# Performance work log

Hardware: AMD Instinct MI355X
Metric: run time of the kernel (lower is better)

## Reference

```python
import jax, jax.numpy as jnp
import numpy as np

# CUBA-LIF constants (from LavaNetwork.__init__ with beta=0.95)
THRESHOLD = 1.0
CURRENT_DECAY = 1.0   # current[t] = (1-1.0)*current[t-1] + input[t] == input[t]
VOLTAGE_DECAY = 1.0 - 0.95  # = 0.05, so v[t] = 0.95*v[t-1] + cur[t]

N_INPUT, N_HIDDEN, N_OUTPUT = 512, 2048, 4 * 64
B, T = 32, 1024


def setup_inputs() -> dict:
    key = jax.random.key(0)
    kx, k1, k2, k3, k4 = jax.random.split(key, 5)
    x = (jax.random.uniform(kx, (B, N_INPUT, T)) < 0.1).astype(jnp.float32)
    # learned params (Linear with bias); small scale so spiking is reasonable
    w1 = jax.random.normal(k1, (N_HIDDEN, N_INPUT), dtype=jnp.float32) * (1.0 / np.sqrt(N_INPUT))
    b1 = jax.random.normal(k2, (N_HIDDEN,), dtype=jnp.float32) * 0.01
    w2 = jax.random.normal(k3, (N_OUTPUT, N_HIDDEN), dtype=jnp.float32) * (1.0 / np.sqrt(N_HIDDEN))
    b2 = jax.random.normal(k4, (N_OUTPUT,), dtype=jnp.float32) * 0.01
    return {"x": x, "w1": w1, "b1": b1, "w2": w2, "b2": b2}


def _cuba_lif(cur):
    """CUBA neuron with current_decay=1 (current==synaptic input),
    leaky-integrate voltage, fire at threshold, reset voltage to 0.
    cur: (B, N, T) -> spikes (B, N, T)."""
    beta_v = 1.0 - VOLTAGE_DECAY  # 0.95

    def step(v, c_t):
        v = v * beta_v + c_t
        s = (v >= THRESHOLD).astype(v.dtype)
        v = v * (1.0 - s)  # reset-to-zero on spike (Loihi behavior)
        return v, s

    cur_t = jnp.moveaxis(cur, -1, 0)  # (T, B, N)
    v0 = jnp.zeros(cur.shape[:-1], cur.dtype)
    _, spk = jax.lax.scan(step, v0, cur_t)
    return jnp.moveaxis(spk, 0, -1)  # (B, N, T)


def reference(x, w1, b1, w2, b2):
    # layer 1: synapse (einsum 'bit,oi->bot' + bias) -> CUBA neuron
    cur1 = jnp.einsum('bit,oi->bot', x, w1) + b1[None, :, None]
    spk1 = _cuba_lif(cur1)
    # layer 2
    cur2 = jnp.einsum('bit,oi->bot', spk1, w2) + b2[None, :, None]
    spk2 = _cuba_lif(cur2)
    return (spk1, spk2)
```

## Files before the change

### kernel.cpp

```cpp
#include <hip/hip_runtime.h>


typedef int i32x4 __attribute__((ext_vector_type(4)));
typedef _Float16 f16x8 __attribute__((ext_vector_type(8)));
typedef _Float16 f16x4 __attribute__((ext_vector_type(4)));
typedef float f32x4 __attribute__((ext_vector_type(4)));

#define GLDS(g, l) __builtin_amdgcn_global_load_lds( \
    (const __attribute__((address_space(1))) void*)(g), \
    (__attribute__((address_space(3))) void*)(l), 16, 0, 0)

#define INV231 4.656612873077392578125e-10


__global__ __launch_bounds__(256) void prep_w8(const float* __restrict__ A,
                                               signed char* __restrict__ wp,
                                               int M, int K)
{
    long gt = (long)blockIdx.x * 256 + threadIdx.x;
    int kq4 = K >> 2;
    int m = (int)(gt / kq4), kq = (int)(gt % kq4);
    int k0 = kq * 4;
    int kt = k0 >> 6, kin = k0 & 63;
    int cw = ((kin >> 4) ^ (m >> 1)) & 3;
    float4 w = *(const float4*)&A[(long)m * K + k0];
    float wv[4] = {w.x, w.y, w.z, w.w};
    int pack[4] = {0, 0, 0, 0};
#pragma unroll
    for (int e = 0; e < 4; e++) {
        long k64 = (long)rint((double)wv[e] * 2147483648.0);
#pragma unroll
        for (int j = 0; j < 3; j++) {
            long r = ((k64 + 128) & 255) - 128;
            pack[j] |= ((int)r & 255) << (e * 8);
            k64 = (k64 - r) >> 8;
        }
        pack[3] |= ((int)k64 & 255) << (e * 8);
    }
#pragma unroll
    for (int p = 0; p < 4; p++)
        *(int*)&wp[(((long)kt * 4 + p) * M + m) * 64 + cw * 16 + (kin & 15)] = pack[p];
}

__global__ __launch_bounds__(256) void prep_x8(const float* __restrict__ x,
                                               unsigned char* __restrict__ xt)
{
    __shared__ float xs[64][68];
    const int b = blockIdx.z, i0 = blockIdx.y * 64, t0 = blockIdx.x * 64;
    const float* xb = x + ((long)b * 512 + i0) * 1024 + t0;
#pragma unroll
    for (int p = 0; p < 4; p++) {
        int f = threadIdx.x + p * 256;
        int i = f >> 4, t4 = (f & 15) * 4;
        *(float4*)&xs[i][t4] = *(const float4*)&xb[(long)i * 1024 + t4];
    }
    __syncthreads();
    int tt = threadIdx.x >> 2, c = threadIdx.x & 3;
    unsigned char bytes[16];
#pragma unroll
    for (int j = 0; j < 16; j++)
        bytes[j] = (unsigned char)xs[c * 16 + j][tt];
    *(uint4*)&xt[(((long)b * 8 + (i0 >> 6)) * 1024 + t0 + tt) * 64 + c * 16] =
        *(uint4*)bytes;
}

__global__ __launch_bounds__(192, 2) void gemm_lif1(
    const signed char* __restrict__ wp,
    const unsigned char* __restrict__ act,
    const float* __restrict__ bias,
    unsigned* __restrict__ mask_ws)
{
    __shared__ signed char Ws[8][4][16][64];
    __shared__ float cs[2][128][17];

    const int m0 = blockIdx.x * 16, b = blockIdx.y;
    const int tid = threadIdx.x, lane = tid & 63, wave = tid >> 6;
    const int lm = lane & 15, lq = lane >> 4;
    const int fro = ((lq ^ (lm >> 1)) & 3) * 16;
    const unsigned char* ab = act + (long)b * 8 * 1024 * 64;

    i32x4 areg[2][4];
    double bv0 = 0.0;

    if (wave < 2) {
        const int gl_row = lane >> 2, gl_col = (lane & 3) * 16;
#pragma unroll
        for (int j = 0; j < 16; ++j) {
            const int r = wave + 2 * j;
            const int kt = r >> 2, p = r & 3;
            const signed char* g = wp + ((long)r * 2048 + m0 + gl_row) * 64 + gl_col;
            GLDS(g, &Ws[kt][p][0][0]);
        }
        bv0 = (double)bias[m0 + lm];
#pragma unroll
        for (int f = 0; f < 4; f++)
            areg[0][f] = *(const i32x4*)
                &ab[((long)(wave * 64 + f * 16 + lm)) * 64 + lq * 16];
    }
    __syncthreads();

    double u = 0.0;
    bool sprev = false;

    for (int p = 0; p < 9; ++p) {
        if (wave < 2 && p < 8) {
            i32x4 acc[4][4];
#pragma unroll
            for (int pp = 0; pp < 4; pp++)
#pragma unroll
                for (int f = 0; f < 4; f++) acc[pp][f] = (i32x4)0;

#pragma unroll
            for (int kk = 0; kk < 8; ++kk) {
                {
                    int pn = p, kn = kk + 1;
                    if (kn == 8) { kn = 0; pn = p + 1; if (pn > 7) { pn = 7; kn = 7; } }
                    const long tt = (long)pn * 128 + wave * 64 + lm;
#pragma unroll
                    for (int f = 0; f < 4; f++)
                        areg[(kk + 1) & 1][f] = *(const i32x4*)
                            &ab[((long)kn * 1024 + tt + f * 16) * 64 + lq * 16];
                }
#pragma unroll
                for (int pp = 0; pp < 4; pp++) {
                    i32x4 w0 = *(const i32x4*)&Ws[kk][pp][lm][fro];
#pragma unroll
                    for (int f = 0; f < 4; f++)
                        acc[pp][f] = __builtin_amdgcn_mfma_i32_16x16x64_i8(
                            areg[kk & 1][f], w0, acc[pp][f], 0, 0, 0);
                }
            }
            const int tb = wave * 64;
#pragma unroll
            for (int tf = 0; tf < 4; tf++)
#pragma unroll
                for (int r = 0; r < 4; r++) {
                    long T = acc[3][tf][r];
                    T = T * 256 + acc[2][tf][r];
                    T = T * 256 + acc[1][tf][r];
                    T = T * 256 + acc[0][tf][r];
                    cs[p & 1][tb + tf * 16 + lq * 4 + r][lm] =
                        (float)((double)T * INV231 + bv0);
                }
        }
        if (wave == 2 && p >= 1 && lane < 16) {
            const int pq = p - 1, buf = pq & 1;
#pragma unroll 1
            for (int g = 0; g < 4; ++g) {
                unsigned mword = 0;
#pragma unroll
                for (int j = 0; j < 32; ++j) {
                    double c = (double)cs[buf][g * 32 + j][lane];
                    double a = 0.95 * u + c;
                    u = sprev ? c : a;
                    bool s = (u >= 1.0);
                    mword |= (s ? 1u : 0u) << j;
                    sprev = s;
                }
                mask_ws[((long)b * 32 + pq * 4 + g) * 2048 + m0 + lane] = mword;
            }
        }
        __syncthreads();
    }
}


__global__ __launch_bounds__(256) void expand_spk8(
    const unsigned* __restrict__ mask_ws,
    unsigned char* __restrict__ spk8)
{
    __shared__ unsigned msk[64][33];
    const int b = blockIdx.x, kt = blockIdx.y;
    const int tid = threadIdx.x;
#pragma unroll
    for (int i = 0; i < 8; ++i) {
        int idx = tid + i * 256;
        int tw = idx >> 6, m = idx & 63;
        msk[m][tw] = mask_ws[((long)b * 32 + tw) * 2048 + kt * 64 + m];
    }
    __syncthreads();
    unsigned char* dst = spk8 + ((long)b * 32 + kt) * 1024 * 64;
#pragma unroll
    for (int i = 0; i < 16; ++i) {
        int off = tid + i * 256;
        int t = off >> 2, mq = off & 3;
        int tw = t >> 5, sh = t & 31;
        unsigned w0 = 0, w1 = 0, w2 = 0, w3 = 0;
#pragma unroll
        for (int j = 0; j < 4; ++j) {
            w0 |= ((msk[mq * 16 + j][tw] >> sh) & 1u) << (8 * j);
            w1 |= ((msk[mq * 16 + 4 + j][tw] >> sh) & 1u) << (8 * j);
            w2 |= ((msk[mq * 16 + 8 + j][tw] >> sh) & 1u) << (8 * j);
            w3 |= ((msk[mq * 16 + 12 + j][tw] >> sh) & 1u) << (8 * j);
        }
        *(uint4*)&dst[(long)off * 16] = (uint4){w0, w1, w2, w3};
    }
}

__global__ __launch_bounds__(256) void expand_spk(
    const unsigned* __restrict__ mask_ws,
    float* __restrict__ spk1)
{
    __shared__ unsigned msk[8][32];
    const long rowbase = (long)blockIdx.x * 8;
    const int b = (int)(rowbase >> 11), m0 = (int)(rowbase & 2047);
    const int tid = threadIdx.x;
    {
        int w = tid >> 3, r = tid & 7;
        msk[r][w] = mask_ws[((long)b * 32 + w) * 2048 + m0 + r];
    }
    __syncthreads();
    const int r = tid >> 5, l5 = tid & 31;
    float* dst = spk1 + (rowbase + r) * 1024;
    const int sh = (l5 & 7) * 4;
#pragma unroll
    for (int j = 0; j < 8; j++) {
        const int t = l5 * 4 + j * 128;
        const unsigned w = msk[r][(l5 >> 3) + j * 4];
        float4 o;
        o.x = ((w >> sh) & 1u) ? 1.f : 0.f;
        o.y = ((w >> (sh + 1)) & 1u) ? 1.f : 0.f;
        o.z = ((w >> (sh + 2)) & 1u) ? 1.f : 0.f;
        o.w = ((w >> (sh + 3)) & 1u) ? 1.f : 0.f;
        *(float4*)&dst[t] = o;
    }
}

template <bool TRANS, int NITER, int CHUNK>
__global__ __launch_bounds__(256, 2) void gemm_i8(
    const signed char* __restrict__ wp,
    const unsigned char* __restrict__ act,
    const float* __restrict__ bias,
    float* __restrict__ C,
    int M)
{
    constexpr int NCHUNK = NITER / CHUNK;
    __shared__ signed char Ws[CHUNK][4][32][64];

    const int b = blockIdx.y;
    const int m0 = blockIdx.z * 32, t0 = blockIdx.x * 256;
    const int tid = threadIdx.x, lane = tid & 63, wave = tid >> 6;
    const int wt = t0 + wave * 64;
    const int lm = lane & 15, lq = lane >> 4;
    const int fro = ((lq ^ (lm >> 1)) & 3) * 16;
    const int gl_row = lane >> 2, gl_col = (lane & 3) * 16;

    const unsigned char* ab = act + (long)b * NITER * 1024 * 64;

    auto stage = [&](int cc) {
#pragma unroll
        for (int j = 0; j < CHUNK; ++j) {
            const int r = wave + 4 * j;
            const int kt = r >> 2, p = r & 3;
            const long kg = ((long)(cc * CHUNK + kt) * 4 + p);
            const signed char* g = wp + (kg * M + m0 + gl_row) * 64 + gl_col;
            GLDS(g, &Ws[kt][p][0][0]);
            GLDS(g + 16 * 64, &Ws[kt][p][16][0]);
        }
    };

    i32x4 acc[4][8];
#pragma unroll
    for (int p = 0; p < 4; p++)
#pragma unroll
        for (int q = 0; q < 8; q++) acc[p][q] = (i32x4)0;

    stage(0);
    i32x4 areg[2][4];
#pragma unroll
    for (int f = 0; f < 4; f++)
        areg[0][f] = *(const i32x4*)&ab[((long)(wt + f * 16 + lm)) * 64 + lq * 16];
    __syncthreads();

    for (int c = 0; c < NCHUNK; ++c) {
#pragma unroll
        for (int kk = 0; kk < CHUNK; ++kk) {
            {
                const int itv = c * CHUNK + kk;
                const long nx = (itv + 1 < NITER) ? itv + 1 : itv;
#pragma unroll
                for (int f = 0; f < 4; f++)
                    areg[(kk + 1) & 1][f] = *(const i32x4*)
                        &ab[(nx * 1024 + wt + f * 16 + lm) * 64 + lq * 16];
            }
#pragma unroll
            for (int p = 0; p < 4; p++) {
                i32x4 w0 = *(const i32x4*)&Ws[kk][p][lm][fro];
                i32x4 w1 = *(const i32x4*)&Ws[kk][p][16 + lm][fro];
                if (TRANS) {
#pragma unroll
                    for (int f = 0; f < 4; f++) {
                        acc[p][f * 2 + 0] = __builtin_amdgcn_mfma_i32_16x16x64_i8(
                            areg[kk & 1][f], w0, acc[p][f * 2 + 0], 0, 0, 0);
                        acc[p][f * 2 + 1] = __builtin_amdgcn_mfma_i32_16x16x64_i8(
                            areg[kk & 1][f], w1, acc[p][f * 2 + 1], 0, 0, 0);
                    }
                } else {
#pragma unroll
                    for (int f = 0; f < 4; f++) {
                        acc[p][0 + f] = __builtin_amdgcn_mfma_i32_16x16x64_i8(
                            w0, areg[kk & 1][f], acc[p][0 + f], 0, 0, 0);
                        acc[p][4 + f] = __builtin_amdgcn_mfma_i32_16x16x64_i8(
                            w1, areg[kk & 1][f], acc[p][4 + f], 0, 0, 0);
                    }
                }
            }
        }
        if (c + 1 < NCHUNK) {
            __syncthreads();
            stage(c + 1);
            __syncthreads();
        }
    }

    if (TRANS) {
        double bv[2];
        bv[0] = (double)bias[m0 + lm];
        bv[1] = (double)bias[m0 + 16 + lm];
        float* Cb = C + (long)b * 1024 * M;
#pragma unroll
        for (int tf = 0; tf < 4; tf++)
#pragma unroll
            for (int r = 0; r < 4; r++) {
                const int trow = wt + tf * 16 + lq * 4 + r;
#pragma unroll
                for (int mf = 0; mf < 2; mf++) {
                    long T = acc[3][tf * 2 + mf][r];
                    T = T * 256 + acc[2][tf * 2 + mf][r];
                    T = T * 256 + acc[1][tf * 2 + mf][r];
                    T = T * 256 + acc[0][tf * 2 + mf][r];
                    Cb[(long)trow * M + m0 + mf * 16 + lm] =
                        (float)((double)T * INV231 + bv[mf]);
                }
            }
    } else {
        float* Cb = C + (long)b * M * 1024;
#pragma unroll
        for (int mf = 0; mf < 2; mf++)
#pragma unroll
            for (int r = 0; r < 4; r++) {
                const int mrow = m0 + mf * 16 + lq * 4 + r;
                const double bv = (double)bias[mrow];
#pragma unroll
                for (int tf = 0; tf < 4; tf++) {
                    long T = acc[3][mf * 4 + tf][r];
                    T = T * 256 + acc[2][mf * 4 + tf][r];
                    T = T * 256 + acc[1][mf * 4 + tf][r];
                    T = T * 256 + acc[0][mf * 4 + tf][r];
                    Cb[(long)mrow * 1024 + wt + tf * 16 + lm] =
                        (float)((double)T * INV231 + bv);
                }
            }
    }
}

template <int RPB>
__global__ __launch_bounds__(256) void lif_lds(float* __restrict__ cur)
{
    __shared__ float cs[RPB][36];
    const long rowbase = (long)blockIdx.x * RPB;
    float* base = cur + rowbase * 1024;
    const int tid = threadIdx.x;
    double v = 0.0;
    const int NV = RPB * 32 / 4;
    for (int tc = 0; tc < 1024; tc += 32) {
        for (int f = tid; f < NV; f += 256) {
            int row = f >> 3, t4 = (f & 7) * 4;
            *(float4*)&cs[row][t4] = *(const float4*)&base[(long)row * 1024 + tc + t4];
        }
        __syncthreads();
        if (tid < RPB) {
#pragma unroll
            for (int j = 0; j < 32; j++) {
                v = 0.95 * v + (double)cs[tid][j];
                bool s = v >= 1.0;
                cs[tid][j] = s ? 1.f : 0.f;
                if (s) v = 0.0;
            }
        }
        __syncthreads();
        for (int f = tid; f < NV; f += 256) {
            int row = f >> 3, t4 = (f & 7) * 4;
            *(float4*)&base[(long)row * 1024 + tc + t4] = *(float4*)&cs[row][t4];
        }
        __syncthreads();
    }
}


__device__ inline void split3(float w, _Float16& q0, _Float16& q1, _Float16& q2) {
    float p0 = rintf(w * 4096.f) * 2.44140625e-4f;
    float r1 = w - p0;
    float p1s = rintf(r1 * 8388608.f) * 2.44140625e-4f;
    float r2 = r1 - p1s * 4.8828125e-4f;
    float p2s = rintf(r2 * 1.7179869184e10f) * 1.220703125e-4f;
    q0 = (_Float16)p0; q1 = (_Float16)p1s; q2 = (_Float16)p2s;
}

__global__ __launch_bounds__(256) void gemm_f16x3_kernel(
    const float* __restrict__ A, const float* __restrict__ Bmat,
    const float* __restrict__ bias, float* __restrict__ C,
    int M, int N, int K, long sB, long sC)
{
    __shared__ _Float16 As[3][128][40];
    __shared__ _Float16 Bsh[128][40];
    const int batch = blockIdx.z;
    const float* Bp = Bmat + (long)batch * sB;
    float* Cp = C + (long)batch * sC;
    const int m0 = blockIdx.y * 128, n0 = blockIdx.x * 128;
    const int tid = threadIdx.x, lane = tid & 63, wave = tid >> 6;
    const int wrow = (wave >> 1) * 64, wcol = (wave & 1) * 64;
    const int lm = lane & 15, lq = lane >> 4;
    const int a_mo = tid >> 3, a_kc = (tid & 7) * 4;
    const int b_kq = tid >> 5, b_nq = tid & 31;

    f32x4 acc[3][4][4];
#pragma unroll
    for (int p = 0; p < 3; p++)
#pragma unroll
        for (int i = 0; i < 4; i++)
#pragma unroll
            for (int j = 0; j < 4; j++) acc[p][i][j] = (f32x4)0.f;

    for (int k0 = 0; k0 < K; k0 += 32) {
#pragma unroll
        for (int i = 0; i < 4; i++) {
            const int m = i * 32 + a_mo;
            float4 w = *(const float4*)&A[(long)(m0 + m) * K + k0 + a_kc];
            _Float16 a0[4], a1[4], a2[4];
            split3(w.x, a0[0], a1[0], a2[0]);
            split3(w.y, a0[1], a1[1], a2[1]);
            split3(w.z, a0[2], a1[2], a2[2]);
            split3(w.w, a0[3], a1[3], a2[3]);
            *(f16x4*)&As[0][m][a_kc] = (f16x4){a0[0], a0[1], a0[2], a0[3]};
            *(f16x4*)&As[1][m][a_kc] = (f16x4){a1[0], a1[1], a1[2], a1[3]};
            *(f16x4*)&As[2][m][a_kc] = (f16x4){a2[0], a2[1], a2[2], a2[3]};
        }
        {
            float4 r0 = *(const float4*)&Bp[(long)(k0 + b_kq * 4 + 0) * N + n0 + b_nq * 4];
            float4 r1 = *(const float4*)&Bp[(long)(k0 + b_kq * 4 + 1) * N + n0 + b_nq * 4];
            float4 r2 = *(const float4*)&Bp[(long)(k0 + b_kq * 4 + 2) * N + n0 + b_nq * 4];
            float4 r3 = *(const float4*)&Bp[(long)(k0 + b_kq * 4 + 3) * N + n0 + b_nq * 4];
            *(f16x4*)&Bsh[b_nq * 4 + 0][b_kq * 4] =
                (f16x4){(_Float16)r0.x, (_Float16)r1.x, (_Float16)r2.x, (_Float16)r3.x};
            *(f16x4*)&Bsh[b_nq * 4 + 1][b_kq * 4] =
                (f16x4){(_Float16)r0.y, (_Float16)r1.y, (_Float16)r2.y, (_Float16)r3.y};
            *(f16x4*)&Bsh[b_nq * 4 + 2][b_kq * 4] =
                (f16x4){(_Float16)r0.z, (_Float16)r1.z, (_Float16)r2.z, (_Float16)r3.z};
            *(f16x4*)&Bsh[b_nq * 4 + 3][b_kq * 4] =
                (f16x4){(_Float16)r0.w, (_Float16)r1.w, (_Float16)r2.w, (_Float16)r3.w};
        }
        __syncthreads();
        f16x8 bf[4];
#pragma unroll
        for (int j = 0; j < 4; j++)
            bf[j] = *(const f16x8*)&Bsh[wcol + j * 16 + lm][lq * 8];
#pragma unroll
        for (int p = 0; p < 3; p++) {
            f16x8 af[4];
#pragma unroll
            for (int i = 0; i < 4; i++)
                af[i] = *(const f16x8*)&As[p][wrow + i * 16 + lm][lq * 8];
#pragma unroll
            for (int i = 0; i < 4; i++)
#pragma unroll
                for (int j = 0; j < 4; j++)
                    acc[p][i][j] = __builtin_amdgcn_mfma_f32_16x16x32_f16(
                        af[i], bf[j], acc[p][i][j], 0, 0, 0);
        }
        __syncthreads();
    }
#pragma unroll
    for (int i = 0; i < 4; i++)
#pragma unroll
        for (int r = 0; r < 4; r++) {
            const int row = m0 + wrow + i * 16 + lq * 4 + r;
            const double bv = (double)bias[row];
#pragma unroll
            for (int j = 0; j < 4; j++) {
                double s = (double)acc[0][i][j][r]
                         + (double)acc[1][i][j][r] * 4.8828125e-4
                         + (double)acc[2][i][j][r] * 4.76837158203125e-7 + bv;
                Cp[(long)row * N + n0 + wcol + j * 16 + lm] = (float)s;
            }
        }
}

__global__ __launch_bounds__(256) void lif_rows(float* __restrict__ data,
                                                long nrows, int T)
{
    long r = (long)blockIdx.x * blockDim.x + threadIdx.x;
    if (r >= nrows) return;
    float* p = data + r * (long)T;
    double v = 0.0;
    for (int t = 0; t < T; t += 4) {
        float4 c = *(float4*)(p + t);
        float4 s;
        v = 0.95 * v + (double)c.x; s.x = (v >= 1.0) ? 1.f : 0.f; if (v >= 1.0) v = 0.0;
        v = 0.95 * v + (double)c.y; s.y = (v >= 1.0) ? 1.f : 0.f; if (v >= 1.0) v = 0.0;
        v = 0.95 * v + (double)c.z; s.z = (v >= 1.0) ? 1.f : 0.f; if (v >= 1.0) v = 0.0;
        v = 0.95 * v + (double)c.w; s.w = (v >= 1.0) ? 1.f : 0.f; if (v >= 1.0) v = 0.0;
        *(float4*)(p + t) = s;
    }
}


extern "C" void kernel_launch(void* const* d_in, const int* in_sizes, int n_in,
                              void* d_out, int out_size, void* d_ws, size_t ws_size,
                              hipStream_t stream)
{
    const float* x  = (const float*)d_in[0];
    const float* w1 = (const float*)d_in[1];
    const float* b1 = (const float*)d_in[2];
    const float* w2 = (const float*)d_in[3];
    const float* b2 = (const float*)d_in[4];

    float* out  = (float*)d_out;
    float* spk1 = out;
    float* spk2 = out + (long)32 * 2048 * 1024;

    const size_t WP1 = 4194304;
    const size_t WP2 = 2097152;
    const size_t X8T = 16777216;
    const size_t SPK = 67108864;
    const size_t MSK = 8388608;
    const size_t NEED = WP1 + WP2 + X8T + SPK + MSK;

    if (ws_size >= NEED) {
        char* ws = (char*)d_ws;
        signed char* wp1 = (signed char*)ws;
        signed char* wp2 = (signed char*)(ws + WP1);
        unsigned char* x8t = (unsigned char*)(ws + WP1 + WP2);
        unsigned char* spk8 = (unsigned char*)(ws + WP1 + WP2 + X8T);
        unsigned* mask_ws = (unsigned*)(ws + WP1 + WP2 + X8T + SPK);

        prep_w8<<<1024, 256, 0, stream>>>(w1, wp1, 2048, 512);
        prep_w8<<<512, 256, 0, stream>>>(w2, wp2, 256, 2048);
        prep_x8<<<dim3(16, 8, 32), 256, 0, stream>>>(x, x8t);

        gemm_lif1<<<dim3(128, 32), 192, 0, stream>>>(wp1, x8t, b1, mask_ws);
        expand_spk8<<<dim3(32, 32), 256, 0, stream>>>(mask_ws, spk8);

        gemm_i8<false, 32, 8><<<dim3(4, 32, 8), 256, 0, stream>>>(
            wp2, spk8, b2, spk2, 256);
        lif_lds<32><<<256, 256, 0, stream>>>(spk2);

        expand_spk<<<8192, 256, 0, stream>>>(mask_ws, spk1);
    } else {
        gemm_f16x3_kernel<<<dim3(8, 16, 32), 256, 0, stream>>>(
            w1, x, b1, spk1, 2048, 1024, 512, (long)512 * 1024, (long)2048 * 1024);
        lif_rows<<<(65536 + 255) / 256, 256, 0, stream>>>(spk1, 65536, 1024);
        gemm_f16x3_kernel<<<dim3(8, 2, 32), 256, 0, stream>>>(
            w2, spk1, b2, spk2, 256, 1024, 2048, (long)2048 * 1024, (long)256 * 1024);
        lif_rows<<<(8192 + 255) / 256, 256, 0, stream>>>(spk2, 8192, 1024);
    }
}
```

Before: 658.9 us.

## Widen fused GEMM+LIF tile to 64 neurons and batch LDS reads in scan

The fused layer-1 GEMM+LIF kernel now covers 64 output neurons per block instead of 16. Four MMA waves each own 16 neurons over 64-step time chunks, and one full wave runs the LIF scan for all 64 neurons. This cuts redundant activation loads across blocks and puts all 64 lanes to work in the scan wave, where before only 16 were active. The cost is a smaller grid (1024 blocks at one block per CU), more LDS per block and twice as many serialized chunk iterations. The LIF loops also preload a row chunk into registers before the sequential dependency chain.

```diff
diff --git a/kernel.cpp b/kernel.cpp
--- a/kernel.cpp
+++ b/kernel.cpp
@@ -64,46 +64,48 @@
         *(uint4*)bytes;
 }
 
-__global__ __launch_bounds__(192, 2) void gemm_lif1(
+__global__ __launch_bounds__(320, 1) void gemm_lif1(
     const signed char* __restrict__ wp,
     const unsigned char* __restrict__ act,
     const float* __restrict__ bias,
     unsigned* __restrict__ mask_ws)
 {
-    __shared__ signed char Ws[8][4][16][64];
-    __shared__ float cs[2][128][17];
-
-    const int m0 = blockIdx.x * 16, b = blockIdx.y;
+    __shared__ signed char Ws[8][4][64][64];
+    __shared__ float cs[2][64][64];
+
+    const int m0 = blockIdx.x * 64, b = blockIdx.y;
     const int tid = threadIdx.x, lane = tid & 63, wave = tid >> 6;
     const int lm = lane & 15, lq = lane >> 4;
     const int fro = ((lq ^ (lm >> 1)) & 3) * 16;
     const unsigned char* ab = act + (long)b * 8 * 1024 * 64;
 
     i32x4 areg[2][4];
-    double bv0 = 0.0;
-
-    if (wave < 2) {
+    double bv = 0.0;
+
+    if (wave < 4) {
         const int gl_row = lane >> 2, gl_col = (lane & 3) * 16;
 #pragma unroll
-        for (int j = 0; j < 16; ++j) {
-            const int r = wave + 2 * j;
-            const int kt = r >> 2, p = r & 3;
+        for (int j = 0; j < 8; ++j) {
+            const int r = wave + 4 * j;
+            const int kt = r >> 2, pl = r & 3;
             const signed char* g = wp + ((long)r * 2048 + m0 + gl_row) * 64 + gl_col;
-            GLDS(g, &Ws[kt][p][0][0]);
-        }
-        bv0 = (double)bias[m0 + lm];
+#pragma unroll
+            for (int q = 0; q < 4; ++q)
+                GLDS(g + q * 16 * 64, &Ws[kt][pl][q * 16][0]);
+        }
+        bv = (double)bias[m0 + wave * 16 + lm];
 #pragma unroll
         for (int f = 0; f < 4; f++)
             areg[0][f] = *(const i32x4*)
-                &ab[((long)(wave * 64 + f * 16 + lm)) * 64 + lq * 16];
+                &ab[((long)(f * 16 + lm)) * 64 + lq * 16];
     }
     __syncthreads();
 
     double u = 0.0;
     bool sprev = false;
 
-    for (int p = 0; p < 9; ++p) {
-        if (wave < 2 && p < 8) {
+    for (int p = 0; p < 17; ++p) {
+        if (wave < 4 && p < 16) {
             i32x4 acc[4][4];
 #pragma unroll
             for (int pp = 0; pp < 4; pp++)
@@ -114,23 +116,22 @@
             for (int kk = 0; kk < 8; ++kk) {
                 {
                     int pn = p, kn = kk + 1;
-                    if (kn == 8) { kn = 0; pn = p + 1; if (pn > 7) { pn = 7; kn = 7; } }
-                    const long tt = (long)pn * 128 + wave * 64 + lm;
+                    if (kn == 8) { kn = 0; pn = p + 1; if (pn > 15) { pn = 15; kn = 7; } }
+                    const long tt = (long)pn * 64 + lm;
 #pragma unroll
                     for (int f = 0; f < 4; f++)
                         areg[(kk + 1) & 1][f] = *(const i32x4*)
                             &ab[((long)kn * 1024 + tt + f * 16) * 64 + lq * 16];
                 }
 #pragma unroll
-                for (int pp = 0; pp < 4; pp++) {
-                    i32x4 w0 = *(const i32x4*)&Ws[kk][pp][lm][fro];
+                for (int pl = 0; pl < 4; pl++) {
+                    i32x4 w0 = *(const i32x4*)&Ws[kk][pl][wave * 16 + lm][fro];
 #pragma unroll
                     for (int f = 0; f < 4; f++)
-                        acc[pp][f] = __builtin_amdgcn_mfma_i32_16x16x64_i8(
-                            areg[kk & 1][f], w0, acc[pp][f], 0, 0, 0);
-                }
-            }
-            const int tb = wave * 64;
+                        acc[pl][f] = __builtin_amdgcn_mfma_i32_16x16x64_i8(
+                            areg[kk & 1][f], w0, acc[pl][f], 0, 0, 0);
+                }
+            }
 #pragma unroll
             for (int tf = 0; tf < 4; tf++)
 #pragma unroll
@@ -139,25 +140,42 @@
                     T = T * 256 + acc[2][tf][r];
                     T = T * 256 + acc[1][tf][r];
                     T = T * 256 + acc[0][tf][r];
-                    cs[p & 1][tb + tf * 16 + lq * 4 + r][lm] =
-                        (float)((double)T * INV231 + bv0);
-                }
-        }
-        if (wave == 2 && p >= 1 && lane < 16) {
+                    cs[p & 1][tf * 16 + lq * 4 + r][wave * 16 + lm] =
+                        (float)((double)T * INV231 + bv);
+                }
+        }
+        if (wave == 4 && p >= 1) {
             const int pq = p - 1, buf = pq & 1;
-#pragma unroll 1
-            for (int g = 0; g < 4; ++g) {
+            float cvA[32], cvB[32];
+#pragma unroll
+            for (int j = 0; j < 32; ++j) cvA[j] = cs[buf][j][lane];
+#pragma unroll
+            for (int j = 0; j < 32; ++j) cvB[j] = cs[buf][32 + j][lane];
+            {
                 unsigned mword = 0;
 #pragma unroll
                 for (int j = 0; j < 32; ++j) {
-                    double c = (double)cs[buf][g * 32 + j][lane];
+                    double c = (double)cvA[j];
                     double a = 0.95 * u + c;
                     u = sprev ? c : a;
                     bool s = (u >= 1.0);
                     mword |= (s ? 1u : 0u) << j;
                     sprev = s;
                 }
-                mask_ws[((long)b * 32 + pq * 4 + g) * 2048 + m0 + lane] = mword;
+                mask_ws[((long)b * 32 + pq * 2 + 0) * 2048 + m0 + lane] = mword;
+            }
+            {
+                unsigned mword = 0;
+#pragma unroll
+                for (int j = 0; j < 32; ++j) {
+                    double c = (double)cvB[j];
+                    double a = 0.95 * u + c;
+                    u = sprev ? c : a;
+                    bool s = (u >= 1.0);
+                    mword |= (s ? 1u : 0u) << j;
+                    sprev = s;
+                }
+                mask_ws[((long)b * 32 + pq * 2 + 1) * 2048 + m0 + lane] = mword;
             }
         }
         __syncthreads();
@@ -370,9 +388,12 @@
         }
         __syncthreads();
         if (tid < RPB) {
+            float cv[32];
+#pragma unroll
+            for (int j = 0; j < 32; j++) cv[j] = cs[tid][j];
 #pragma unroll
             for (int j = 0; j < 32; j++) {
-                v = 0.95 * v + (double)cs[tid][j];
+                v = 0.95 * v + (double)cv[j];
                 bool s = v >= 1.0;
                 cs[tid][j] = s ? 1.f : 0.f;
                 if (s) v = 0.0;
@@ -538,7 +559,7 @@
         prep_w8<<<512, 256, 0, stream>>>(w2, wp2, 256, 2048);
         prep_x8<<<dim3(16, 8, 32), 256, 0, stream>>>(x, x8t);
 
-        gemm_lif1<<<dim3(128, 32), 192, 0, stream>>>(wp1, x8t, b1, mask_ws);
+        gemm_lif1<<<dim3(32, 32), 320, 0, stream>>>(wp1, x8t, b1, mask_ws);
         expand_spk8<<<dim3(32, 32), 256, 0, stream>>>(mask_ws, spk8);
 
         gemm_i8<false, 32, 8><<<dim3(4, 32, 8), 256, 0, stream>>>(
```

After: 638.4 us. -3.1%, faster.
